# Performance work log

Hardware: AMD Instinct MI355X
Metric: run time of the kernel (lower is better)

The kernel has to match this reference:

```python
import jax, jax.numpy as jnp
import numpy as np

N, K, H, F = 100000, 32, 3, 6  # nodes, neighbors per node, heads, emb channels per head
HF = H * F                      # 18
EPS = 1e-5


def batch_norm(x, gamma, beta):
    # BatchNorm1d in training mode: batch statistics, biased variance
    mu = x.mean(0)
    var = x.var(0)
    return (x - mu) / jnp.sqrt(var + EPS) * gamma + beta


def mha_layer(x, edge_index, W, b, attW, attb, e_feats=None):
    xe = x @ W + b                                   # [N, H*F]
    src = xe[edge_index[0]].reshape(N, K, H, F)      # gather source node feats
    drn = xe[edge_index[1]].reshape(N, K, H, F)      # gather drain node feats
    if e_feats is not None:
        ef = jnp.broadcast_to(e_feats.reshape(N, K, 1, -1), (N, K, H, e_feats.shape[-1]))
        cat = jnp.concatenate([src, drn, ef], axis=3)
    else:
        cat = jnp.concatenate([src, drn], axis=3)
    scores = (cat @ attW + attb)[..., 0]             # [N, K, H]; activation=Identity
    att = jax.nn.softmax(scores, axis=1)             # softmax over the K neighbors
    y = jnp.einsum('nkh,nkhf->nhf', att, src) / K    # head_agg='cat'
    return y.reshape(N, HF)


def setup_inputs() -> dict:
    key = jax.random.key(0)
    ks = jax.random.split(key, 16)
    s = 0.1
    inp = {
        'x': jax.random.normal(ks[0], (N, 1), dtype=jnp.float32),
        'edge_index': jax.random.randint(ks[1], (2, N * K), 0, N, dtype=jnp.int32),
        'e': jax.random.normal(ks[2], (N * K, 2), dtype=jnp.float32),
        # conv0: in=1, att in = 2*6 + 2 = 14
        'W0': s * jax.random.normal(ks[3], (1, HF), dtype=jnp.float32),
        'b0': jnp.zeros((HF,), jnp.float32),
        'aW0': s * jax.random.normal(ks[4], (14, 1), dtype=jnp.float32),
        'ab0': jnp.zeros((1,), jnp.float32),
        # conv1: in=1+18=19, att in = 12
        'W1': s * jax.random.normal(ks[5], (19, HF), dtype=jnp.float32),
        'b1': jnp.zeros((HF,), jnp.float32),
        'aW1': s * jax.random.normal(ks[6], (12, 1), dtype=jnp.float32),
        'ab1': jnp.zeros((1,), jnp.float32),
        # conv2: in=1+18+18=37, att in = 12
        'W2': s * jax.random.normal(ks[7], (37, HF), dtype=jnp.float32),
        'b2': jnp.zeros((HF,), jnp.float32),
        'aW2': s * jax.random.normal(ks[8], (12, 1), dtype=jnp.float32),
        'ab2': jnp.zeros((1,), jnp.float32),
        # batch norms
        'g0': jnp.ones((1,), jnp.float32), 'be0': jnp.zeros((1,), jnp.float32),
        'g1': jnp.ones((HF,), jnp.float32), 'be1': jnp.zeros((HF,), jnp.float32),
        'g2': jnp.ones((HF,), jnp.float32), 'be2': jnp.zeros((HF,), jnp.float32),
        'g3': jnp.ones((HF,), jnp.float32), 'be3': jnp.zeros((HF,), jnp.float32),
        # final fc
        'fW': s * jax.random.normal(ks[9], (HF, 1), dtype=jnp.float32),
        'fb': jnp.zeros((1,), jnp.float32),
    }
    return inp


def reference(x, edge_index, e, W0, b0, aW0, ab0, W1, b1, aW1, ab1,
              W2, b2, aW2, ab2, g0, be0, g1, be1, g2, be2, g3, be3, fW, fb):
    x0 = batch_norm(x, g0, be0)                                  # [N,1]
    x1 = mha_layer(x0, edge_index, W0, b0, aW0, ab0, e_feats=e)  # [N,18]
    x1 = batch_norm(x1, g1, be1)
    x1 = jnp.concatenate([x0, x1], axis=1)                       # [N,19]
    x2 = mha_layer(x1, edge_index, W1, b1, aW1, ab1)             # [N,18]
    x2 = batch_norm(x2, g2, be2)
    x2 = jnp.concatenate([x1, x2], axis=1)                       # [N,37]
    y = mha_layer(x2, edge_index, W2, b2, aW2, ab2)              # [N,18]
    y = batch_norm(y, g3, be3)
    return y @ fW + fb                                           # [N,1]
```

## Files before the change

kernel.cpp:

```cpp
#include <hip/hip_runtime.h>
#include <hip/hip_fp16.h>

#define N_NODES 100000
#define KN 32
#define EPS 1e-5f
#define NSLOT 128

#define OFF_X0   0
#define OFF_XEH  500000
#define OFF_S4   2500000
#define OFF_X2   2900000
#define OFF_Y    4700000
#define OFF_TX   6500000
#define OFF_SS   6500016
#define OFF_X2S  6501040
#define OFF_YS   6505648
#define OFF_P    6510256

__device__ inline float2 h2f2(unsigned int w) {
    __half2 h = *reinterpret_cast<__half2*>(&w);
    return __half22float2(h);
}

__global__ __launch_bounds__(256)
void statsx_kernel(const float4* __restrict__ x4, float* __restrict__ acc) {
    int i = blockIdx.x * 256 + threadIdx.x;
    float s = 0.f, ss = 0.f;
    if (i < 25000) {
        float4 v = x4[i];
        s = v.x + v.y + v.z + v.w;
        ss = v.x * v.x + v.y * v.y + v.z * v.z + v.w * v.w;
    }
#pragma unroll
    for (int off = 32; off > 0; off >>= 1) {
        s  += __shfl_xor(s,  off, 64);
        ss += __shfl_xor(ss, off, 64);
    }
    __shared__ float ls[4], lss[4];
    int wid = threadIdx.x >> 6;
    if ((threadIdx.x & 63) == 0) { ls[wid] = s; lss[wid] = ss; }
    __syncthreads();
    if (threadIdx.x == 0) {
        atomicAdd(&acc[0], ls[0] + ls[1] + ls[2] + ls[3]);
        atomicAdd(&acc[1], lss[0] + lss[1] + lss[2] + lss[3]);
    }
}

__global__ void prep0_kernel(const float* __restrict__ T, float* __restrict__ P,
                             const float* g0, const float* be0,
                             const float* W0, const float* b0,
                             const float* aW0, const float* ab0) {
    if (threadIdx.x || blockIdx.x) return;
    float mu  = T[0] / (float)N_NODES;
    float var = T[1] / (float)N_NODES - mu * mu;
    float inv = rsqrtf(var + EPS);
    float s0 = inv * g0[0];
    P[0] = s0; P[1] = be0[0] - mu * s0;
    for (int h = 0; h < 3; ++h) {
        float A = 0.f, B = 0.f, Cc = 0.f;
        for (int f = 0; f < 6; ++f) {
            A  = fmaf(W0[h * 6 + f], aW0[f], A);
            B  = fmaf(W0[h * 6 + f], aW0[6 + f], B);
            Cc = fmaf(b0[h * 6 + f], aW0[f] + aW0[6 + f], Cc);
        }
        P[2 + h] = A; P[5 + h] = B; P[8 + h] = Cc + ab0[0];
    }
    P[11] = aW0[12]; P[12] = aW0[13];
}

__global__ void x0_kernel(const float4* __restrict__ x4, const float* __restrict__ P,
                          float4* __restrict__ x0) {
    int i = blockIdx.x * blockDim.x + threadIdx.x;
    if (i < 25000) {
        float4 v = x4[i];
        float s = P[0], t = P[1];
        x0[i] = make_float4(fmaf(v.x, s, t), fmaf(v.y, s, t), fmaf(v.z, s, t), fmaf(v.w, s, t));
    }
}

__global__ __launch_bounds__(256)
void att0_kernel(const float* __restrict__ x0,
                 const int* __restrict__ ei0, const int* __restrict__ ei1,
                 const float2* __restrict__ e2,
                 const float* __restrict__ P, float4* __restrict__ S4,
                 float* __restrict__ SS) {
    int hw = threadIdx.x >> 5;
    int node = blockIdx.x * 8 + hw;
    int k = threadIdx.x & 31;
    int eidx = node * KN + k;
    int s = ei0[eidx], d = ei1[eidx];
    float xs = x0[s], xd = x0[d];
    float2 ef = e2[eidx];
    float eb = fmaf(ef.x, P[11], ef.y * P[12]);
    float sc0 = fmaf(xs, P[2], fmaf(xd, P[5], P[8]  + eb));
    float sc1 = fmaf(xs, P[3], fmaf(xd, P[6], P[9]  + eb));
    float sc2 = fmaf(xs, P[4], fmaf(xd, P[7], P[10] + eb));
    float m0 = sc0, m1 = sc1, m2 = sc2;
#pragma unroll
    for (int off = 16; off > 0; off >>= 1) {
        m0 = fmaxf(m0, __shfl_xor(m0, off, 32));
        m1 = fmaxf(m1, __shfl_xor(m1, off, 32));
        m2 = fmaxf(m2, __shfl_xor(m2, off, 32));
    }
    float w0 = __expf(sc0 - m0), w1 = __expf(sc1 - m1), w2 = __expf(sc2 - m2);
    float l0 = w0, l1 = w1, l2 = w2;
    float a0 = w0 * xs, a1 = w1 * xs, a2 = w2 * xs;
#pragma unroll
    for (int off = 16; off > 0; off >>= 1) {
        l0 += __shfl_xor(l0, off, 32); a0 += __shfl_xor(a0, off, 32);
        l1 += __shfl_xor(l1, off, 32); a1 += __shfl_xor(a1, off, 32);
        l2 += __shfl_xor(l2, off, 32); a2 += __shfl_xor(a2, off, 32);
    }
    __shared__ float sS[8][4];
    if (k == 0) {
        float v0 = a0 / l0, v1 = a1 / l1, v2 = a2 / l2;
        S4[node] = make_float4(v0, v1, v2, 0.f);
        sS[hw][0] = v0; sS[hw][1] = v1; sS[hw][2] = v2;
    }
    __syncthreads();
    if (threadIdx.x < 3) {
        float ps = 0.f, pss = 0.f;
#pragma unroll
        for (int h = 0; h < 8; ++h) { float v = sS[h][threadIdx.x]; ps += v; pss = fmaf(v, v, pss); }
        int slot = (blockIdx.x & (NSLOT - 1)) * 8;
        atomicAdd(&SS[slot + threadIdx.x], ps);
        atomicAdd(&SS[slot + 4 + threadIdx.x], pss);
    }
}

__global__ void prep1_kernel(const float* __restrict__ SS, float* __restrict__ P,
                             const float* W0, const float* g1, const float* be1,
                             const float* W1, const float* b1) {
    __shared__ float muS[3], varS[3], alpha[18], beta[18];
    int t = threadIdx.x;
    if (t < 3) {
        float s = 0.f, ss = 0.f;
#pragma unroll 8
        for (int i = 0; i < NSLOT; ++i) { s += SS[i * 8 + t]; ss += SS[i * 8 + 4 + t]; }
        float mu = s / (float)N_NODES;
        muS[t] = mu; varS[t] = ss / (float)N_NODES - mu * mu;
    }
    __syncthreads();
    if (t < 18) {
        int h = t / 6;
        float w = W0[t] / (float)KN;
        float inv1 = rsqrtf(varS[h] * w * w + EPS);
        float gg = inv1 * g1[t];
        alpha[t] = w * gg;
        beta[t]  = be1[t] - w * gg * muS[h];
    }
    __syncthreads();
    if (t < 18) {
        int j = t;
        float* M1 = P + 16; float* c1 = P + 88;
        M1[j] = W1[j];
        for (int h = 0; h < 3; ++h) {
            float acc = 0.f;
            for (int f = 0; f < 6; ++f) acc = fmaf(alpha[h * 6 + f], W1[(1 + h * 6 + f) * 18 + j], acc);
            M1[(1 + h) * 18 + j] = acc;
        }
        float cc = b1[j];
        for (int c = 0; c < 18; ++c) cc = fmaf(beta[c], W1[(1 + c) * 18 + j], cc);
        c1[j] = cc;
    }
}

__device__ inline void pack_row(unsigned short* __restrict__ xeh, int n,
                                const float* row, float q0, float q1, float q2) {
    union { unsigned short u[24]; uint4 v[3]; } pk;
#pragma unroll
    for (int j = 0; j < 18; ++j) pk.u[j] = __half_as_ushort(__float2half(row[j]));
    pk.u[18] = 0; pk.u[19] = 0;
    pk.u[20] = __half_as_ushort(__float2half(q0));
    pk.u[21] = __half_as_ushort(__float2half(q1));
    pk.u[22] = __half_as_ushort(__float2half(q2));
    pk.u[23] = 0;
    uint4* dst = (uint4*)(xeh + (size_t)n * 24);
    dst[0] = pk.v[0]; dst[1] = pk.v[1]; dst[2] = pk.v[2];
}

__global__ void xe1_kernel(const float* __restrict__ x0, const float4* __restrict__ S4,
                           const float* __restrict__ P, const float* __restrict__ aW1,
                           unsigned short* __restrict__ xeh) {
    int n = blockIdx.x * blockDim.x + threadIdx.x;
    if (n >= N_NODES) return;
    float xv = x0[n];
    float4 S = S4[n];
    const float* M1 = P + 16; const float* c1 = P + 88;
    float row[18];
#pragma unroll
    for (int j = 0; j < 18; ++j) {
        float r = c1[j];
        r = fmaf(xv,  M1[j],      r);
        r = fmaf(S.x, M1[18 + j], r);
        r = fmaf(S.y, M1[36 + j], r);
        r = fmaf(S.z, M1[54 + j], r);
        row[j] = r;
    }
    float q0 = 0.f, q1 = 0.f, q2 = 0.f;
#pragma unroll
    for (int f = 0; f < 6; ++f) {
        float a = aW1[6 + f];
        q0 = fmaf(row[f], a, q0);
        q1 = fmaf(row[6 + f], a, q1);
        q2 = fmaf(row[12 + f], a, q2);
    }
    pack_row(xeh, n, row, q0, q1, q2);
}

__global__ __launch_bounds__(256)
void att_big_kernel(const unsigned short* __restrict__ xeh,
                    const int* __restrict__ ei0, const int* __restrict__ ei1,
                    const float* __restrict__ aW, const float* __restrict__ abp,
                    float* __restrict__ out, float* __restrict__ slots) {
    int hw = threadIdx.x >> 5;
    int node = blockIdx.x * 8 + hw;
    int k = threadIdx.x & 31;
    int eidx = node * KN + k;
    int s = ei0[eidx], d = ei1[eidx];
    const unsigned short* rs = xeh + (size_t)s * 24;
    uint4 A = *(const uint4*)rs;
    uint4 B = *(const uint4*)(rs + 8);
    unsigned int C = *(const unsigned int*)(rs + 16);
    uint2 Q = *(const uint2*)(xeh + (size_t)d * 24 + 20);
    float2 p01 = h2f2(A.x), p23 = h2f2(A.y), p45 = h2f2(A.z), p67 = h2f2(A.w);
    float2 p89 = h2f2(B.x), pab = h2f2(B.y), pcd = h2f2(B.z), pef = h2f2(B.w);
    float2 pgh = h2f2(C);
    float2 q01 = h2f2(Q.x), q2_ = h2f2(Q.y);
    float r[18];
    r[0]=p01.x; r[1]=p01.y; r[2]=p23.x; r[3]=p23.y; r[4]=p45.x; r[5]=p45.y;
    r[6]=p67.x; r[7]=p67.y; r[8]=p89.x; r[9]=p89.y; r[10]=pab.x; r[11]=pab.y;
    r[12]=pcd.x; r[13]=pcd.y; r[14]=pef.x; r[15]=pef.y; r[16]=pgh.x; r[17]=pgh.y;
    float a0 = aW[0], a1 = aW[1], a2 = aW[2], a3 = aW[3], a4 = aW[4], a5 = aW[5];
    float ab = abp[0];
    float sc0 = fmaf(r[0],a0, fmaf(r[1],a1, fmaf(r[2],a2, fmaf(r[3],a3, fmaf(r[4],a4, r[5]*a5))))) + q01.x + ab;
    float sc1 = fmaf(r[6],a0, fmaf(r[7],a1, fmaf(r[8],a2, fmaf(r[9],a3, fmaf(r[10],a4, r[11]*a5))))) + q01.y + ab;
    float sc2 = fmaf(r[12],a0, fmaf(r[13],a1, fmaf(r[14],a2, fmaf(r[15],a3, fmaf(r[16],a4, r[17]*a5))))) + q2_.x + ab;
    float m0 = sc0, m1 = sc1, m2 = sc2;
#pragma unroll
    for (int off = 16; off > 0; off >>= 1) {
        m0 = fmaxf(m0, __shfl_xor(m0, off, 32));
        m1 = fmaxf(m1, __shfl_xor(m1, off, 32));
        m2 = fmaxf(m2, __shfl_xor(m2, off, 32));
    }
    float w0 = __expf(sc0 - m0), w1 = __expf(sc1 - m1), w2 = __expf(sc2 - m2);
    float l0 = w0, l1 = w1, l2 = w2;
    float v[18];
#pragma unroll
    for (int j = 0; j < 6; ++j) {
        v[j]      = w0 * r[j];
        v[6 + j]  = w1 * r[6 + j];
        v[12 + j] = w2 * r[12 + j];
    }
#pragma unroll
    for (int off = 16; off > 0; off >>= 1) {
        l0 += __shfl_xor(l0, off, 32);
        l1 += __shfl_xor(l1, off, 32);
        l2 += __shfl_xor(l2, off, 32);
#pragma unroll
        for (int j = 0; j < 18; ++j) v[j] += __shfl_xor(v[j], off, 32);
    }
    __shared__ float so[8][18];
    if (k == 0) {
        float i0 = 1.f / (l0 * (float)KN);
        float i1 = 1.f / (l1 * (float)KN);
        float i2 = 1.f / (l2 * (float)KN);
        size_t base = (size_t)node * 18;
#pragma unroll
        for (int j = 0; j < 6; ++j) {
            float o0 = v[j] * i0, o1 = v[6 + j] * i1, o2 = v[12 + j] * i2;
            out[base + j] = o0;      so[hw][j] = o0;
            out[base + 6 + j] = o1;  so[hw][6 + j] = o1;
            out[base + 12 + j] = o2; so[hw][12 + j] = o2;
        }
    }
    __syncthreads();
    if (threadIdx.x < 18) {
        int t = threadIdx.x;
        float ps = 0.f, pss = 0.f;
#pragma unroll
        for (int h = 0; h < 8; ++h) { float vv = so[h][t]; ps += vv; pss = fmaf(vv, vv, pss); }
        int slot = (blockIdx.x & (NSLOT - 1)) * 36;
        atomicAdd(&slots[slot + t], ps);
        atomicAdd(&slots[slot + 18 + t], pss);
    }
}

__global__ void prep2_kernel(const float* __restrict__ SS, const float* __restrict__ X2S,
                             float* __restrict__ P,
                             const float* W0, const float* g1, const float* be1,
                             const float* g2, const float* be2,
                             const float* W2, const float* b2) {
    __shared__ float muS[3], varS[3], alpha[18], beta[18], gam[18], del[18];
    int t = threadIdx.x;
    if (t < 3) {
        float s = 0.f, ss = 0.f;
#pragma unroll 8
        for (int i = 0; i < NSLOT; ++i) { s += SS[i * 8 + t]; ss += SS[i * 8 + 4 + t]; }
        float mu = s / (float)N_NODES;
        muS[t] = mu; varS[t] = ss / (float)N_NODES - mu * mu;
    }
    if (t < 18) {
        float s = 0.f, ss = 0.f;
#pragma unroll 8
        for (int i = 0; i < NSLOT; ++i) { s += X2S[i * 36 + t]; ss += X2S[i * 36 + 18 + t]; }
        float mu2 = s / (float)N_NODES;
        float var2 = ss / (float)N_NODES - mu2 * mu2;
        float g = rsqrtf(var2 + EPS) * g2[t];
        gam[t] = g; del[t] = be2[t] - mu2 * g;
    }
    __syncthreads();
    if (t < 18) {
        int h = t / 6;
        float w = W0[t] / (float)KN;
        float inv1 = rsqrtf(varS[h] * w * w + EPS);
        float gg = inv1 * g1[t];
        alpha[t] = w * gg;
        beta[t]  = be1[t] - w * gg * muS[h];
    }
    __syncthreads();
    if (t < 18) {
        int j = t;
        float* M2 = P + 112; float* c2 = P + 508;
        M2[j] = W2[j];
        for (int h = 0; h < 3; ++h) {
            float acc = 0.f;
            for (int f = 0; f < 6; ++f) acc = fmaf(alpha[h * 6 + f], W2[(1 + h * 6 + f) * 18 + j], acc);
            M2[(1 + h) * 18 + j] = acc;
        }
        for (int c = 0; c < 18; ++c) M2[(4 + c) * 18 + j] = gam[c] * W2[(19 + c) * 18 + j];
        float cc = b2[j];
        for (int c = 0; c < 18; ++c) cc = fmaf(beta[c], W2[(1 + c) * 18 + j], cc);
        for (int c = 0; c < 18; ++c) cc = fmaf(del[c],  W2[(19 + c) * 18 + j], cc);
        c2[j] = cc;
    }
}

__global__ void xe2_kernel(const float* __restrict__ x0, const float4* __restrict__ S4,
                           const float* __restrict__ x2, const float* __restrict__ P,
                           const float* __restrict__ aW2,
                           unsigned short* __restrict__ xeh) {
    int n = blockIdx.x * blockDim.x + threadIdx.x;
    if (n >= N_NODES) return;
    float xv = x0[n];
    float4 S = S4[n];
    float xr[18];
    const float2* x2p = (const float2*)(x2 + (size_t)n * 18);
#pragma unroll
    for (int q = 0; q < 9; ++q) { float2 v = x2p[q]; xr[2 * q] = v.x; xr[2 * q + 1] = v.y; }
    const float* M2 = P + 112; const float* c2 = P + 508;
    float row[18];
#pragma unroll
    for (int j = 0; j < 18; ++j) {
        float r = c2[j];
        r = fmaf(xv,  M2[j],      r);
        r = fmaf(S.x, M2[18 + j], r);
        r = fmaf(S.y, M2[36 + j], r);
        r = fmaf(S.z, M2[54 + j], r);
#pragma unroll
        for (int c = 0; c < 18; ++c) r = fmaf(xr[c], M2[(4 + c) * 18 + j], r);
        row[j] = r;
    }
    float q0 = 0.f, q1 = 0.f, q2 = 0.f;
#pragma unroll
    for (int f = 0; f < 6; ++f) {
        float a = aW2[6 + f];
        q0 = fmaf(row[f], a, q0);
        q1 = fmaf(row[6 + f], a, q1);
        q2 = fmaf(row[12 + f], a, q2);
    }
    pack_row(xeh, n, row, q0, q1, q2);
}

__global__ void prepF_kernel(const float* __restrict__ YS, float* __restrict__ P,
                             const float* g3, const float* be3,
                             const float* fW, const float* fb) {
    __shared__ float part[18];
    int t = threadIdx.x;
    if (t < 18) {
        float s = 0.f, ss = 0.f;
#pragma unroll 8
        for (int i = 0; i < NSLOT; ++i) { s += YS[i * 36 + t]; ss += YS[i * 36 + 18 + t]; }
        float mu = s / (float)N_NODES;
        float var = ss / (float)N_NODES - mu * mu;
        float g = rsqrtf(var + EPS) * g3[t];
        P[528 + t] = g * fW[t];
        part[t] = (be3[t] - mu * g) * fW[t];
    }
    __syncthreads();
    if (t == 0) {
        float cf = fb[0];
        for (int j = 0; j < 18; ++j) cf += part[j];
        P[546] = cf;
    }
}

__global__ __launch_bounds__(256)
void final_kernel(const float4* __restrict__ y4, const float* __restrict__ P,
                  float2* __restrict__ out2) {
    int i = blockIdx.x * blockDim.x + threadIdx.x;
    if (i >= 50000) return;
    const float4* yp = y4 + (size_t)i * 9;
    float a[36];
#pragma unroll
    for (int q = 0; q < 9; ++q) {
        float4 v = yp[q];
        a[4 * q] = v.x; a[4 * q + 1] = v.y; a[4 * q + 2] = v.z; a[4 * q + 3] = v.w;
    }
    float cf = P[546];
    float acc0 = cf, acc1 = cf;
#pragma unroll
    for (int j = 0; j < 18; ++j) {
        float w = P[528 + j];
        acc0 = fmaf(a[j], w, acc0);
        acc1 = fmaf(a[18 + j], w, acc1);
    }
    out2[i] = make_float2(acc0, acc1);
}

extern "C" void kernel_launch(void* const* d_in, const int* in_sizes, int n_in,
                              void* d_out, int out_size, void* d_ws, size_t ws_size,
                              hipStream_t stream) {
    const float* x   = (const float*)d_in[0];
    const int*   ei  = (const int*)d_in[1];
    const float* e   = (const float*)d_in[2];
    const float* W0  = (const float*)d_in[3];
    const float* b0  = (const float*)d_in[4];
    const float* aW0 = (const float*)d_in[5];
    const float* ab0 = (const float*)d_in[6];
    const float* W1  = (const float*)d_in[7];
    const float* b1  = (const float*)d_in[8];
    const float* aW1 = (const float*)d_in[9];
    const float* ab1 = (const float*)d_in[10];
    const float* W2  = (const float*)d_in[11];
    const float* b2  = (const float*)d_in[12];
    const float* aW2 = (const float*)d_in[13];
    const float* ab2 = (const float*)d_in[14];
    const float* g0  = (const float*)d_in[15];
    const float* be0 = (const float*)d_in[16];
    const float* g1  = (const float*)d_in[17];
    const float* be1 = (const float*)d_in[18];
    const float* g2  = (const float*)d_in[19];
    const float* be2 = (const float*)d_in[20];
    const float* g3  = (const float*)d_in[21];
    const float* be3 = (const float*)d_in[22];
    const float* fW  = (const float*)d_in[23];
    const float* fb  = (const float*)d_in[24];

    const int* ei0 = ei;
    const int* ei1 = ei + (size_t)N_NODES * KN;

    float*  ws  = (float*)d_ws;
    float*  x0  = ws + OFF_X0;
    unsigned short* xeh = (unsigned short*)(ws + OFF_XEH);
    float4* S4  = (float4*)(ws + OFF_S4);
    float*  x2  = ws + OFF_X2;
    float*  y   = ws + OFF_Y;
    float*  TX  = ws + OFF_TX;
    float*  SS  = ws + OFF_SS;
    float*  X2S = ws + OFF_X2S;
    float*  YS  = ws + OFF_YS;
    float*  P   = ws + OFF_P;

    hipMemsetAsync(TX, 0, (OFF_P - OFF_TX) * sizeof(float), stream);

    statsx_kernel<<<98, 256, 0, stream>>>((const float4*)x, TX);
    prep0_kernel<<<1, 1, 0, stream>>>(TX, P, g0, be0, W0, b0, aW0, ab0);
    x0_kernel<<<98, 256, 0, stream>>>((const float4*)x, P, (float4*)x0);

    att0_kernel<<<N_NODES / 8, 256, 0, stream>>>(x0, ei0, ei1, (const float2*)e, P, S4, SS);

    prep1_kernel<<<1, 64, 0, stream>>>(SS, P, W0, g1, be1, W1, b1);
    xe1_kernel<<<(N_NODES + 255) / 256, 256, 0, stream>>>(x0, S4, P, aW1, xeh);
    att_big_kernel<<<N_NODES / 8, 256, 0, stream>>>(xeh, ei0, ei1, aW1, ab1, x2, X2S);

    prep2_kernel<<<1, 64, 0, stream>>>(SS, X2S, P, W0, g1, be1, g2, be2, W2, b2);
    xe2_kernel<<<(N_NODES + 255) / 256, 256, 0, stream>>>(x0, S4, x2, P, aW2, xeh);
    att_big_kernel<<<N_NODES / 8, 256, 0, stream>>>(xeh, ei0, ei1, aW2, ab2, y, YS);

    prepF_kernel<<<1, 64, 0, stream>>>(YS, P, g3, be3, fW, fb);
    final_kernel<<<(50000 + 255) / 256, 256, 0, stream>>>((const float4*)y, P, (float2*)d_out);
}
```

Measured before the change: 348.6 us.

## Gather compact 4-dim layer-1 basis instead of full 18-wide projected rows

Layer 1's projected features are a linear function of four per-node values (x0 and the three head sums), so the attention kernel now gathers a 16-byte half-precision record per neighbour holding those values plus the drain score terms. It forms source scores with a precomputed 4x3 matrix, aggregates the four weighted basis values with warp shuffles, and expands to 18 outputs through M1 only once per node. This cuts per-edge gather traffic from a 48-byte row to 16 bytes, at the cost of extra shuffle reductions and storing x0 and S in half precision. prep2 and xe2 are moved in the file with no change to their logic.

Result: faster. 325.3 us (-6.7%).

```diff
diff --git a/kernel.cpp b/kernel.cpp
--- a/kernel.cpp
+++ b/kernel.cpp
@@ -8,6 +8,7 @@
 
 #define OFF_X0   0
 #define OFF_XEH  500000
+#define OFF_Z1Q  1800000
 #define OFF_S4   2500000
 #define OFF_X2   2900000
 #define OFF_Y    4700000
@@ -130,8 +131,9 @@
 
 __global__ void prep1_kernel(const float* __restrict__ SS, float* __restrict__ P,
                              const float* W0, const float* g1, const float* be1,
-                             const float* W1, const float* b1) {
-    __shared__ float muS[3], varS[3], alpha[18], beta[18];
+                             const float* W1, const float* b1,
+                             const float* aW1, const float* ab1) {
+    __shared__ float muS[3], varS[3], alpha[18], beta[18], sM1[4][18], sc1[18];
     int t = threadIdx.x;
     if (t < 3) {
         float s = 0.f, ss = 0.f;
@@ -153,15 +155,190 @@
     if (t < 18) {
         int j = t;
         float* M1 = P + 16; float* c1 = P + 88;
-        M1[j] = W1[j];
+        float m0 = W1[j];
+        sM1[0][j] = m0; M1[j] = m0;
         for (int h = 0; h < 3; ++h) {
             float acc = 0.f;
             for (int f = 0; f < 6; ++f) acc = fmaf(alpha[h * 6 + f], W1[(1 + h * 6 + f) * 18 + j], acc);
-            M1[(1 + h) * 18 + j] = acc;
+            sM1[1 + h][j] = acc; M1[(1 + h) * 18 + j] = acc;
         }
         float cc = b1[j];
         for (int c = 0; c < 18; ++c) cc = fmaf(beta[c], W1[(1 + c) * 18 + j], cc);
-        c1[j] = cc;
+        sc1[j] = cc; c1[j] = cc;
+    }
+    __syncthreads();
+    if (t < 12) {
+        int c = t / 3, h = t - c * 3;
+        float acc = 0.f;
+        for (int f = 0; f < 6; ++f) acc = fmaf(sM1[c][h * 6 + f], aW1[f], acc);
+        P[548 + c * 3 + h] = acc;
+    } else if (t < 15) {
+        int h = t - 12;
+        float acc = ab1[0];
+        for (int f = 0; f < 6; ++f) acc = fmaf(sc1[h * 6 + f], aW1[f], acc);
+        P[560 + h] = acc;
+    }
+}
+
+__global__ void zq1_kernel(const float* __restrict__ x0, const float4* __restrict__ S4,
+                           const float* __restrict__ P, const float* __restrict__ aW1,
+                           uint4* __restrict__ z1q1) {
+    int n = blockIdx.x * blockDim.x + threadIdx.x;
+    if (n >= N_NODES) return;
+    float xv = x0[n];
+    float4 S = S4[n];
+    const float* M1 = P + 16; const float* c1 = P + 88;
+    float row[18];
+#pragma unroll
+    for (int j = 0; j < 18; ++j) {
+        float r = c1[j];
+        r = fmaf(xv,  M1[j],      r);
+        r = fmaf(S.x, M1[18 + j], r);
+        r = fmaf(S.y, M1[36 + j], r);
+        r = fmaf(S.z, M1[54 + j], r);
+        row[j] = r;
+    }
+    float q0 = 0.f, q1 = 0.f, q2 = 0.f;
+#pragma unroll
+    for (int f = 0; f < 6; ++f) {
+        float a = aW1[6 + f];
+        q0 = fmaf(row[f], a, q0);
+        q1 = fmaf(row[6 + f], a, q1);
+        q2 = fmaf(row[12 + f], a, q2);
+    }
+    union { unsigned short u[8]; uint4 v; } pk;
+    pk.u[0] = __half_as_ushort(__float2half(xv));
+    pk.u[1] = __half_as_ushort(__float2half(S.x));
+    pk.u[2] = __half_as_ushort(__float2half(S.y));
+    pk.u[3] = __half_as_ushort(__float2half(S.z));
+    pk.u[4] = __half_as_ushort(__float2half(q0));
+    pk.u[5] = __half_as_ushort(__float2half(q1));
+    pk.u[6] = __half_as_ushort(__float2half(q2));
+    pk.u[7] = 0;
+    z1q1[n] = pk.v;
+}
+
+__global__ __launch_bounds__(256)
+void att_z1_kernel(const uint4* __restrict__ z1q1,
+                   const int* __restrict__ ei0, const int* __restrict__ ei1,
+                   const float* __restrict__ P,
+                   float* __restrict__ out, float* __restrict__ slots) {
+    int hw = threadIdx.x >> 5;
+    int node = blockIdx.x * 8 + hw;
+    int k = threadIdx.x & 31;
+    int eidx = node * KN + k;
+    int s = ei0[eidx], d = ei1[eidx];
+    uint4 Rs = z1q1[s];
+    uint4 Rd = z1q1[d];
+    float2 z01 = h2f2(Rs.x), z23 = h2f2(Rs.y);
+    float zc0 = z01.x, zc1 = z01.y, zc2 = z23.x, zc3 = z23.y;
+    float2 q01 = h2f2(Rd.z), q23 = h2f2(Rd.w);
+    const float* PM = P + 548;
+    const float* pc = P + 560;
+    float sc0 = pc[0] + q01.x, sc1 = pc[1] + q01.y, sc2 = pc[2] + q23.x;
+    sc0 = fmaf(zc0, PM[0], fmaf(zc1, PM[3], fmaf(zc2, PM[6], fmaf(zc3, PM[9],  sc0))));
+    sc1 = fmaf(zc0, PM[1], fmaf(zc1, PM[4], fmaf(zc2, PM[7], fmaf(zc3, PM[10], sc1))));
+    sc2 = fmaf(zc0, PM[2], fmaf(zc1, PM[5], fmaf(zc2, PM[8], fmaf(zc3, PM[11], sc2))));
+    float m0 = sc0, m1 = sc1, m2 = sc2;
+#pragma unroll
+    for (int off = 16; off > 0; off >>= 1) {
+        m0 = fmaxf(m0, __shfl_xor(m0, off, 32));
+        m1 = fmaxf(m1, __shfl_xor(m1, off, 32));
+        m2 = fmaxf(m2, __shfl_xor(m2, off, 32));
+    }
+    float w0 = __expf(sc0 - m0), w1 = __expf(sc1 - m1), w2 = __expf(sc2 - m2);
+    float l0 = w0, l1 = w1, l2 = w2;
+    float A[3][4];
+#pragma unroll
+    for (int c = 0; c < 4; ++c) {
+        float z = (c == 0) ? zc0 : (c == 1) ? zc1 : (c == 2) ? zc2 : zc3;
+        A[0][c] = w0 * z; A[1][c] = w1 * z; A[2][c] = w2 * z;
+    }
+#pragma unroll
+    for (int off = 16; off > 0; off >>= 1) {
+        l0 += __shfl_xor(l0, off, 32);
+        l1 += __shfl_xor(l1, off, 32);
+        l2 += __shfl_xor(l2, off, 32);
+#pragma unroll
+        for (int h = 0; h < 3; ++h)
+#pragma unroll
+            for (int c = 0; c < 4; ++c) A[h][c] += __shfl_xor(A[h][c], off, 32);
+    }
+    __shared__ float so[8][18];
+    if (k < 18) {
+        int t = k;
+        int h = t / 6;
+        float lh = (h == 0) ? l0 : (h == 1) ? l1 : l2;
+        float Ah0 = (h == 0) ? A[0][0] : (h == 1) ? A[1][0] : A[2][0];
+        float Ah1 = (h == 0) ? A[0][1] : (h == 1) ? A[1][1] : A[2][1];
+        float Ah2 = (h == 0) ? A[0][2] : (h == 1) ? A[1][2] : A[2][2];
+        float Ah3 = (h == 0) ? A[0][3] : (h == 1) ? A[1][3] : A[2][3];
+        const float* M1 = P + 16; const float* c1 = P + 88;
+        float acc = Ah0 * M1[t] + Ah1 * M1[18 + t] + Ah2 * M1[36 + t] + Ah3 * M1[54 + t];
+        float inv = 1.f / (lh * (float)KN);
+        float x2v = fmaf(acc, inv, c1[t] * (1.f / (float)KN));
+        out[(size_t)node * 18 + t] = x2v;
+        so[hw][t] = x2v;
+    }
+    __syncthreads();
+    if (threadIdx.x < 18) {
+        int t = threadIdx.x;
+        float ps = 0.f, pss = 0.f;
+#pragma unroll
+        for (int h = 0; h < 8; ++h) { float vv = so[h][t]; ps += vv; pss = fmaf(vv, vv, pss); }
+        int slot = (blockIdx.x & (NSLOT - 1)) * 36;
+        atomicAdd(&slots[slot + t], ps);
+        atomicAdd(&slots[slot + 18 + t], pss);
+    }
+}
+
+__global__ void prep2_kernel(const float* __restrict__ SS, const float* __restrict__ X2S,
+                             float* __restrict__ P,
+                             const float* W0, const float* g1, const float* be1,
+                             const float* g2, const float* be2,
+                             const float* W2, const float* b2) {
+    __shared__ float muS[3], varS[3], alpha[18], beta[18], gam[18], del[18];
+    int t = threadIdx.x;
+    if (t < 3) {
+        float s = 0.f, ss = 0.f;
+#pragma unroll 8
+        for (int i = 0; i < NSLOT; ++i) { s += SS[i * 8 + t]; ss += SS[i * 8 + 4 + t]; }
+        float mu = s / (float)N_NODES;
+        muS[t] = mu; varS[t] = ss / (float)N_NODES - mu * mu;
+    }
+    if (t < 18) {
+        float s = 0.f, ss = 0.f;
+#pragma unroll 8
+        for (int i = 0; i < NSLOT; ++i) { s += X2S[i * 36 + t]; ss += X2S[i * 36 + 18 + t]; }
+        float mu2 = s / (float)N_NODES;
+        float var2 = ss / (float)N_NODES - mu2 * mu2;
+        float g = rsqrtf(var2 + EPS) * g2[t];
+        gam[t] = g; del[t] = be2[t] - mu2 * g;
+    }
+    __syncthreads();
+    if (t < 18) {
+        int h = t / 6;
+        float w = W0[t] / (float)KN;
+        float inv1 = rsqrtf(varS[h] * w * w + EPS);
+        float gg = inv1 * g1[t];
+        alpha[t] = w * gg;
+        beta[t]  = be1[t] - w * gg * muS[h];
+    }
+    __syncthreads();
+    if (t < 18) {
+        int j = t;
+        float* M2 = P + 112; float* c2 = P + 508;
+        M2[j] = W2[j];
+        for (int h = 0; h < 3; ++h) {
+            float acc = 0.f;
+            for (int f = 0; f < 6; ++f) acc = fmaf(alpha[h * 6 + f], W2[(1 + h * 6 + f) * 18 + j], acc);
+            M2[(1 + h) * 18 + j] = acc;
+        }
+        for (int c = 0; c < 18; ++c) M2[(4 + c) * 18 + j] = gam[c] * W2[(19 + c) * 18 + j];
+        float cc = b2[j];
+        for (int c = 0; c < 18; ++c) cc = fmaf(beta[c], W2[(1 + c) * 18 + j], cc);
+        for (int c = 0; c < 18; ++c) cc = fmaf(del[c],  W2[(19 + c) * 18 + j], cc);
+        c2[j] = cc;
     }
 }
 
@@ -179,28 +356,35 @@
     dst[0] = pk.v[0]; dst[1] = pk.v[1]; dst[2] = pk.v[2];
 }
 
-__global__ void xe1_kernel(const float* __restrict__ x0, const float4* __restrict__ S4,
-                           const float* __restrict__ P, const float* __restrict__ aW1,
+__global__ void xe2_kernel(const float* __restrict__ x0, const float4* __restrict__ S4,
+                           const float* __restrict__ x2, const float* __restrict__ P,
+                           const float* __restrict__ aW2,
                            unsigned short* __restrict__ xeh) {
     int n = blockIdx.x * blockDim.x + threadIdx.x;
     if (n >= N_NODES) return;
     float xv = x0[n];
     float4 S = S4[n];
-    const float* M1 = P + 16; const float* c1 = P + 88;
+    float xr[18];
+    const float2* x2p = (const float2*)(x2 + (size_t)n * 18);
+#pragma unroll
+    for (int q = 0; q < 9; ++q) { float2 v = x2p[q]; xr[2 * q] = v.x; xr[2 * q + 1] = v.y; }
+    const float* M2 = P + 112; const float* c2 = P + 508;
     float row[18];
 #pragma unroll
     for (int j = 0; j < 18; ++j) {
-        float r = c1[j];
-        r = fmaf(xv,  M1[j],      r);
-        r = fmaf(S.x, M1[18 + j], r);
-        r = fmaf(S.y, M1[36 + j], r);
-        r = fmaf(S.z, M1[54 + j], r);
+        float r = c2[j];
+        r = fmaf(xv,  M2[j],      r);
+        r = fmaf(S.x, M2[18 + j], r);
+        r = fmaf(S.y, M2[36 + j], r);
+        r = fmaf(S.z, M2[54 + j], r);
+#pragma unroll
+        for (int c = 0; c < 18; ++c) r = fmaf(xr[c], M2[(4 + c) * 18 + j], r);
         row[j] = r;
     }
     float q0 = 0.f, q1 = 0.f, q2 = 0.f;
 #pragma unroll
     for (int f = 0; f < 6; ++f) {
-        float a = aW1[6 + f];
+        float a = aW2[6 + f];
         q0 = fmaf(row[f], a, q0);
         q1 = fmaf(row[6 + f], a, q1);
         q2 = fmaf(row[12 + f], a, q2);
@@ -286,92 +470,6 @@
     }
 }
 
-__global__ void prep2_kernel(const float* __restrict__ SS, const float* __restrict__ X2S,
-                             float* __restrict__ P,
-                             const float* W0, const float* g1, const float* be1,
-                             const float* g2, const float* be2,
-                             const float* W2, const float* b2) {
-    __shared__ float muS[3], varS[3], alpha[18], beta[18], gam[18], del[18];
-    int t = threadIdx.x;
-    if (t < 3) {
-        float s = 0.f, ss = 0.f;
-#pragma unroll 8
-        for (int i = 0; i < NSLOT; ++i) { s += SS[i * 8 + t]; ss += SS[i * 8 + 4 + t]; }
-        float mu = s / (float)N_NODES;
-        muS[t] = mu; varS[t] = ss / (float)N_NODES - mu * mu;
-    }
-    if (t < 18) {
-        float s = 0.f, ss = 0.f;
-#pragma unroll 8
-        for (int i = 0; i < NSLOT; ++i) { s += X2S[i * 36 + t]; ss += X2S[i * 36 + 18 + t]; }
-        float mu2 = s / (float)N_NODES;
-        float var2 = ss / (float)N_NODES - mu2 * mu2;
-        float g = rsqrtf(var2 + EPS) * g2[t];
-        gam[t] = g; del[t] = be2[t] - mu2 * g;
-    }
-    __syncthreads();
-    if (t < 18) {
-        int h = t / 6;
-        float w = W0[t] / (float)KN;
-        float inv1 = rsqrtf(varS[h] * w * w + EPS);
-        float gg = inv1 * g1[t];
-        alpha[t] = w * gg;
-        beta[t]  = be1[t] - w * gg * muS[h];
-    }
-    __syncthreads();
-    if (t < 18) {
-        int j = t;
-        float* M2 = P + 112; float* c2 = P + 508;
-        M2[j] = W2[j];
-        for (int h = 0; h < 3; ++h) {
-            float acc = 0.f;
-            for (int f = 0; f < 6; ++f) acc = fmaf(alpha[h * 6 + f], W2[(1 + h * 6 + f) * 18 + j], acc);
-            M2[(1 + h) * 18 + j] = acc;
-        }
-        for (int c = 0; c < 18; ++c) M2[(4 + c) * 18 + j] = gam[c] * W2[(19 + c) * 18 + j];
-        float cc = b2[j];
-        for (int c = 0; c < 18; ++c) cc = fmaf(beta[c], W2[(1 + c) * 18 + j], cc);
-        for (int c = 0; c < 18; ++c) cc = fmaf(del[c],  W2[(19 + c) * 18 + j], cc);
-        c2[j] = cc;
-    }
-}
-
-__global__ void xe2_kernel(const float* __restrict__ x0, const float4* __restrict__ S4,
-                           const float* __restrict__ x2, const float* __restrict__ P,
-                           const float* __restrict__ aW2,
-                           unsigned short* __restrict__ xeh) {
-    int n = blockIdx.x * blockDim.x + threadIdx.x;
-    if (n >= N_NODES) return;
-    float xv = x0[n];
-    float4 S = S4[n];
-    float xr[18];
-    const float2* x2p = (const float2*)(x2 + (size_t)n * 18);
-#pragma unroll
-    for (int q = 0; q < 9; ++q) { float2 v = x2p[q]; xr[2 * q] = v.x; xr[2 * q + 1] = v.y; }
-    const float* M2 = P + 112; const float* c2 = P + 508;
-    float row[18];
-#pragma unroll
-    for (int j = 0; j < 18; ++j) {
-        float r = c2[j];
-        r = fmaf(xv,  M2[j],      r);
-        r = fmaf(S.x, M2[18 + j], r);
-        r = fmaf(S.y, M2[36 + j], r);
-        r = fmaf(S.z, M2[54 + j], r);
-#pragma unroll
-        for (int c = 0; c < 18; ++c) r = fmaf(xr[c], M2[(4 + c) * 18 + j], r);
-        row[j] = r;
-    }
-    float q0 = 0.f, q1 = 0.f, q2 = 0.f;
-#pragma unroll
-    for (int f = 0; f < 6; ++f) {
-        float a = aW2[6 + f];
-        q0 = fmaf(row[f], a, q0);
-        q1 = fmaf(row[6 + f], a, q1);
-        q2 = fmaf(row[12 + f], a, q2);
-    }
-    pack_row(xeh, n, row, q0, q1, q2);
-}
-
 __global__ void prepF_kernel(const float* __restrict__ YS, float* __restrict__ P,
                              const float* g3, const float* be3,
                              const float* fW, const float* fb) {
@@ -453,6 +551,7 @@
     float*  ws  = (float*)d_ws;
     float*  x0  = ws + OFF_X0;
     unsigned short* xeh = (unsigned short*)(ws + OFF_XEH);
+    uint4*  z1q1 = (uint4*)(ws + OFF_Z1Q);
     float4* S4  = (float4*)(ws + OFF_S4);
     float*  x2  = ws + OFF_X2;
     float*  y   = ws + OFF_Y;
@@ -470,9 +569,9 @@
 
     att0_kernel<<<N_NODES / 8, 256, 0, stream>>>(x0, ei0, ei1, (const float2*)e, P, S4, SS);
 
-    prep1_kernel<<<1, 64, 0, stream>>>(SS, P, W0, g1, be1, W1, b1);
-    xe1_kernel<<<(N_NODES + 255) / 256, 256, 0, stream>>>(x0, S4, P, aW1, xeh);
-    att_big_kernel<<<N_NODES / 8, 256, 0, stream>>>(xeh, ei0, ei1, aW1, ab1, x2, X2S);
+    prep1_kernel<<<1, 64, 0, stream>>>(SS, P, W0, g1, be1, W1, b1, aW1, ab1);
+    zq1_kernel<<<(N_NODES + 255) / 256, 256, 0, stream>>>(x0, S4, P, aW1, z1q1);
+    att_z1_kernel<<<N_NODES / 8, 256, 0, stream>>>(z1q1, ei0, ei1, P, x2, X2S);
 
     prep2_kernel<<<1, 64, 0, stream>>>(SS, X2S, P, W0, g1, be1, g2, be2, W2, b2);
     xe2_kernel<<<(N_NODES + 255) / 256, 256, 0, stream>>>(x0, S4, x2, P, aW2, xeh);
```
